# Kernel tuning notes

Measured on AMD Instinct MI355X. Metric: run time of the kernel, lower is better.

Reference implementation:

```python
import jax, jax.numpy as jnp
import numpy as np

EPS = 1e-5
NEG_SLOPE = 0.2


def batchnorm_nodes(x, gamma, beta):
    # BatchNorm2d over channel=node axis; x: [N, T, D], stats over (T, D) per node
    m = x.mean(axis=(1, 2), keepdims=True)
    v = ((x - m) ** 2).mean(axis=(1, 2), keepdims=True)
    return (x - m) * jax.lax.rsqrt(v + EPS) * gamma[:, None, None] + beta[:, None, None]


def gat_relation(h, src, dst, W, al, ar, N):
    # h: [N, T, D]; W: [D, H, dh]; al/ar: [H, dh]
    z = jnp.einsum('ntd,dhe->nthe', h, W)              # [N, T, H, dh]
    el = jnp.einsum('nthe,he->nth', z, al)             # [N, T, H]
    er = jnp.einsum('nthe,he->nth', z, ar)
    e = jax.nn.leaky_relu(el[src] + er[dst], NEG_SLOPE)  # [E, T, H]
    emax = jax.ops.segment_max(e, dst, num_segments=N)   # [N, T, H]
    ex = jnp.exp(e - emax[dst])
    denom = jax.ops.segment_sum(ex, dst, num_segments=N)
    alpha = ex / jnp.maximum(denom[dst], 1e-16)          # segment softmax over in-edges
    msg = alpha[..., None] * z[src]                      # [E, T, H, dh]
    return jax.ops.segment_sum(msg, dst, num_segments=N)  # [N, T, H, dh]


def setup_inputs() -> dict:
    key = jax.random.key(0)
    ks = jax.random.split(key, 12)
    N, T, D, H, E, DFF = 10000, 12, 64, 4, 100000, 128
    dh = D // H
    s = 0.1
    return {
        'x': jax.random.normal(ks[0], (N, T, D), jnp.float32),
        'src1': jax.random.randint(ks[1], (E,), 0, N, jnp.int32),
        'dst1': jax.random.randint(ks[2], (E,), 0, N, jnp.int32),
        'src2': jax.random.randint(ks[3], (E,), 0, N, jnp.int32),
        'dst2': jax.random.randint(ks[4], (E,), 0, N, jnp.int32),
        'W1': jax.random.normal(ks[5], (D, H, dh), jnp.float32) * s,
        'al1': jax.random.normal(ks[6], (H, dh), jnp.float32) * s,
        'ar1': jax.random.normal(ks[7], (H, dh), jnp.float32) * s,
        'W2': jax.random.normal(ks[8], (D, H, dh), jnp.float32) * s,
        'al2': jax.random.normal(ks[9], (H, dh), jnp.float32) * s,
        'ar2': jax.random.normal(ks[10], (H, dh), jnp.float32) * s,
        'bn1_g': jnp.ones((N,), jnp.float32),
        'bn1_b': jnp.zeros((N,), jnp.float32),
        'bn2_g': jnp.ones((N,), jnp.float32),
        'bn2_b': jnp.zeros((N,), jnp.float32),
        'ff_w1': jax.random.normal(ks[11], (D, DFF), jnp.float32) * s,
        'ff_b1': jnp.zeros((DFF,), jnp.float32),
        'ff_w2': jax.random.normal(jax.random.fold_in(key, 99), (DFF, D), jnp.float32) * s,
        'ff_b2': jnp.zeros((D,), jnp.float32),
    }


def reference(x, src1, dst1, src2, dst2, W1, al1, ar1, W2, al2, ar2,
              bn1_g, bn1_b, bn2_g, bn2_b, ff_w1, ff_b1, ff_w2, ff_b2):
    N, T, D = x.shape
    h = batchnorm_nodes(x, bn1_g, bn1_b)
    # HeteroGraphConv: per-relation GAT, sum aggregation
    m = gat_relation(h, src1, dst1, W1, al1, ar1, N) \
      + gat_relation(h, src2, dst2, W2, al2, ar2, N)   # [N, T, H, dh]
    m = m.reshape(N, T, D)
    x2 = x + m                                          # residual (dropout=identity in eval)
    h2 = batchnorm_nodes(x2, bn2_g, bn2_b)
    ff = jax.nn.gelu(h2 @ ff_w1 + ff_b1, approximate=False) @ ff_w2 + ff_b2
    return x2 + ff
```

## Files before the change

kernel.cpp:

```cpp
#include <hip/hip_runtime.h>
#include <math.h>

constexpr int kT = 12;
constexpr float kNeg = 0.2f;
constexpr float kEps = 1e-5f;
constexpr float kLog2e = 1.44269504088896f;

typedef __attribute__((ext_vector_type(8))) short bf16x8;
typedef __attribute__((ext_vector_type(4))) float f32x4;

__device__ __forceinline__ short f2bf(float f) {
  union { float f; unsigned u; } v;
  v.f = f;
  return (short)((v.u + 0x7fffu + ((v.u >> 16) & 1u)) >> 16);
}
__device__ __forceinline__ unsigned pack2(float a, float b) {
  return (unsigned)(unsigned short)f2bf(a) | ((unsigned)(unsigned short)f2bf(b) << 16);
}

__device__ __forceinline__ float wave_reduce_sum(float v) {
#pragma unroll
  for (int o = 32; o > 0; o >>= 1) v += __shfl_xor(v, o);
  return v;
}

__global__ void bnprep_kernel(const float* __restrict__ x, const float* __restrict__ g,
                              const float* __restrict__ b, float* __restrict__ scale,
                              float* __restrict__ shift, const float* __restrict__ fw1,
                              const float* __restrict__ fw2, const float* __restrict__ zW1,
                              const float* __restrict__ zW2, bf16x8* __restrict__ fw1f,
                              bf16x8* __restrict__ fw2f, bf16x8* __restrict__ zw1f,
                              bf16x8* __restrict__ zw2f, int N) {
  int blk = blockIdx.x;
  int lane = threadIdx.x & 63, wid = threadIdx.x >> 6;
  if (blk >= N) {
    int which = blk - N;
    int m = lane & 15, q = lane >> 4;
    if (which == 0) {
      for (int fi = wid; fi < 16; fi += 4) {
        int mt = fi >> 1, kc = fi & 1;
        bf16x8 v;
#pragma unroll
        for (int j = 0; j < 8; j++) v[j] = f2bf(fw1[(kc * 32 + q * 8 + j) * 128 + mt * 16 + m]);
        fw1f[fi * 64 + lane] = v;
      }
    } else if (which == 1) {
      for (int fi = wid; fi < 16; fi += 4) {
        int mt2 = fi >> 2, kc2 = fi & 3;
        bf16x8 u;
#pragma unroll
        for (int j = 0; j < 8; j++) u[j] = f2bf(fw2[(kc2 * 32 + q * 8 + j) * 64 + mt2 * 16 + m]);
        fw2f[fi * 64 + lane] = u;
      }
    } else if (which == 2) {
      for (int fi = wid; fi < 8; fi += 4) {
        int mt = fi >> 1, kc = fi & 1;
        bf16x8 v;
#pragma unroll
        for (int j = 0; j < 8; j++) v[j] = f2bf(zW1[(kc * 32 + q * 8 + j) * 64 + mt * 16 + m]);
        zw1f[fi * 64 + lane] = v;
      }
    } else {
      for (int fi = wid; fi < 8; fi += 4) {
        int mt = fi >> 1, kc = fi & 1;
        bf16x8 v;
#pragma unroll
        for (int j = 0; j < 8; j++) v[j] = f2bf(zW2[(kc * 32 + q * 8 + j) * 64 + mt * 16 + m]);
        zw2f[fi * 64 + lane] = v;
      }
    }
    return;
  }
  int n = blk;
  const float* xr = x + (size_t)n * (kT * 64);
  float s = 0.f, s2 = 0.f;
  for (int i = threadIdx.x; i < kT * 64; i += blockDim.x) {
    float v = xr[i];
    s += v;
    s2 += v * v;
  }
  s = wave_reduce_sum(s);
  s2 = wave_reduce_sum(s2);
  __shared__ float ls[4], ls2[4];
  if (lane == 0) { ls[wid] = s; ls2[wid] = s2; }
  __syncthreads();
  if (threadIdx.x == 0) {
    float ts = 0.f, ts2 = 0.f;
    for (int i = 0; i < 4; i++) { ts += ls[i]; ts2 += ls2[i]; }
    const float inv = 1.f / (kT * 64);
    float mean = ts * inv;
    float var = ts2 * inv - mean * mean;
    float sc = rsqrtf(var + kEps) * g[n];
    scale[n] = sc;
    shift[n] = b[n] - mean * sc;
  }
}

__global__ void deg_kernel(const int* __restrict__ dst1, const int* __restrict__ dst2,
                           int* __restrict__ deg1, int* __restrict__ deg2, int E1, int E2) {
  int i = blockIdx.x * blockDim.x + threadIdx.x;
  if (i < E1) atomicAdd(&deg1[dst1[i]], 1);
  else if (i < E1 + E2) atomicAdd(&deg2[dst2[i - E1]], 1);
}

__global__ void scan_kernel(const int* __restrict__ deg1, int* __restrict__ off1,
                            const int* __restrict__ deg2, int* __restrict__ off2, int N) {
  const int* deg = blockIdx.x ? deg2 : deg1;
  int* off = blockIdx.x ? off2 : off1;
  __shared__ int wsum[16];
  __shared__ int carry;
  int tid = threadIdx.x, lane = tid & 63, wv = tid >> 6;
  if (tid == 0) { carry = 0; off[0] = 0; }
  __syncthreads();
  for (int base = 0; base < N; base += 1024) {
    int i = base + tid;
    int incl = (i < N) ? deg[i] : 0;
#pragma unroll
    for (int o = 1; o < 64; o <<= 1) {
      int y = __shfl_up(incl, o);
      if (lane >= o) incl += y;
    }
    if (lane == 63) wsum[wv] = incl;
    __syncthreads();
    if (tid < 16) {
      int p = wsum[tid];
#pragma unroll
      for (int o = 1; o < 16; o <<= 1) {
        int y = __shfl_up(p, o);
        if (tid >= o) p += y;
      }
      wsum[tid] = p;
    }
    __syncthreads();
    int prefix = carry + (wv > 0 ? wsum[wv - 1] : 0);
    if (i < N) off[i + 1] = prefix + incl;
    int total = carry + wsum[15];
    __syncthreads();
    if (tid == 0) carry = total;
    __syncthreads();
  }
}

__global__ void fill_kernel(const int* __restrict__ src1, const int* __restrict__ dst1,
                            const int* __restrict__ off1, int* __restrict__ cur1,
                            int* __restrict__ scsr1, const int* __restrict__ src2,
                            const int* __restrict__ dst2, const int* __restrict__ off2,
                            int* __restrict__ cur2, int* __restrict__ scsr2, int E1, int E2) {
  int i = blockIdx.x * blockDim.x + threadIdx.x;
  if (i < E1) {
    int d = dst1[i];
    int p = atomicAdd(&cur1[d], 1);
    scsr1[off1[d] + p] = src1[i] * kT;
  } else if (i < E1 + E2) {
    int k = i - E1;
    int d = dst2[k];
    int p = atomicAdd(&cur2[d], 1);
    scsr2[off2[d] + p] = src2[k] * kT;
  }
}

__global__ __launch_bounds__(256) void zel_kernel(
    const float* __restrict__ x, const float* __restrict__ scale,
    const float* __restrict__ shift, const bf16x8* __restrict__ zw1f,
    const bf16x8* __restrict__ zw2f, const float* __restrict__ al1,
    const float* __restrict__ ar1, const float* __restrict__ al2,
    const float* __restrict__ ar2, unsigned short* __restrict__ z1,
    unsigned short* __restrict__ z2, float* __restrict__ el1, float* __restrict__ er1,
    float* __restrict__ el2, float* __restrict__ er2, int NT) {
  __shared__ bf16x8 sW1[8][64];
  __shared__ bf16x8 sW2[8][64];
  int lane = threadIdx.x & 63, wid = threadIdx.x >> 6;
  int m = lane & 15, q = lane >> 4;
  for (int fi = wid; fi < 8; fi += 4) {
    sW1[fi][lane] = zw1f[fi * 64 + lane];
    sW2[fi][lane] = zw2f[fi * 64 + lane];
  }
  __syncthreads();
  float al1r[4][4], ar1r[4][4], al2r[4][4], ar2r[4][4];
#pragma unroll
  for (int h = 0; h < 4; h++)
#pragma unroll
    for (int r = 0; r < 4; r++) {
      int f = h * 16 + 4 * q + r;
      al1r[h][r] = al1[f] * kLog2e;
      ar1r[h][r] = ar1[f] * kLog2e;
      al2r[h][r] = al2[f] * kLog2e;
      ar2r[h][r] = ar2[f] * kLog2e;
    }
  int ntile = (NT + 15) / 16;
  for (int tile = blockIdx.x * 4 + wid; tile < ntile; tile += gridDim.x * 4) {
    int r0 = tile * 16;
    int row = r0 + m;
    int rowc = (row < NT) ? row : NT - 1;
    int n = rowc / kT;
    float sc = scale[n], sh = shift[n];
    bf16x8 hf[2];
#pragma unroll
    for (int kc = 0; kc < 2; kc++) {
      float4 p0 = *(const float4*)&x[(size_t)rowc * 64 + kc * 32 + q * 8];
      float4 p1 = *(const float4*)&x[(size_t)rowc * 64 + kc * 32 + q * 8 + 4];
      hf[kc][0] = f2bf(fmaf(p0.x, sc, sh));
      hf[kc][1] = f2bf(fmaf(p0.y, sc, sh));
      hf[kc][2] = f2bf(fmaf(p0.z, sc, sh));
      hf[kc][3] = f2bf(fmaf(p0.w, sc, sh));
      hf[kc][4] = f2bf(fmaf(p1.x, sc, sh));
      hf[kc][5] = f2bf(fmaf(p1.y, sc, sh));
      hf[kc][6] = f2bf(fmaf(p1.z, sc, sh));
      hf[kc][7] = f2bf(fmaf(p1.w, sc, sh));
    }
    f32x4 a1[4], a2[4];
#pragma unroll
    for (int mt = 0; mt < 4; mt++) {
      a1[mt] = (f32x4){0.f, 0.f, 0.f, 0.f};
      a2[mt] = (f32x4){0.f, 0.f, 0.f, 0.f};
    }
#pragma unroll
    for (int kc = 0; kc < 2; kc++)
#pragma unroll
      for (int mt = 0; mt < 4; mt++) {
        a1[mt] = __builtin_amdgcn_mfma_f32_16x16x32_bf16(sW1[mt * 2 + kc][lane], hf[kc],
                                                         a1[mt], 0, 0, 0);
        a2[mt] = __builtin_amdgcn_mfma_f32_16x16x32_bf16(sW2[mt * 2 + kc][lane], hf[kc],
                                                         a2[mt], 0, 0, 0);
      }
    float e1l[4], e1r[4], e2l[4], e2r[4];
#pragma unroll
    for (int h = 0; h < 4; h++) {
      float pl1 = 0.f, pr1 = 0.f, pl2 = 0.f, pr2 = 0.f;
#pragma unroll
      for (int r = 0; r < 4; r++) {
        pl1 = fmaf(a1[h][r], al1r[h][r], pl1);
        pr1 = fmaf(a1[h][r], ar1r[h][r], pr1);
        pl2 = fmaf(a2[h][r], al2r[h][r], pl2);
        pr2 = fmaf(a2[h][r], ar2r[h][r], pr2);
      }
#pragma unroll
      for (int o = 16; o < 64; o <<= 1) {
        pl1 += __shfl_xor(pl1, o);
        pr1 += __shfl_xor(pr1, o);
        pl2 += __shfl_xor(pl2, o);
        pr2 += __shfl_xor(pr2, o);
      }
      e1l[h] = pl1; e1r[h] = pr1; e2l[h] = pl2; e2r[h] = pr2;
    }
    if (row < NT) {
      if (q == 0) {
        *(float4*)&el1[(size_t)row * 4] = make_float4(e1l[0], e1l[1], e1l[2], e1l[3]);
        *(float4*)&er1[(size_t)row * 4] = make_float4(e1r[0], e1r[1], e1r[2], e1r[3]);
        *(float4*)&el2[(size_t)row * 4] = make_float4(e2l[0], e2l[1], e2l[2], e2l[3]);
        *(float4*)&er2[(size_t)row * 4] = make_float4(e2r[0], e2r[1], e2r[2], e2r[3]);
      }
#pragma unroll
      for (int mt = 0; mt < 4; mt++) {
        uint2 u1 = {pack2(a1[mt][0], a1[mt][1]), pack2(a1[mt][2], a1[mt][3])};
        uint2 u2 = {pack2(a2[mt][0], a2[mt][1]), pack2(a2[mt][2], a2[mt][3])};
        *(uint2*)&z1[(size_t)row * 64 + mt * 16 + 4 * q] = u1;
        *(uint2*)&z2[(size_t)row * 64 + mt * 16 + 4 * q] = u2;
      }
    }
  }
}

__device__ __forceinline__ void gat_rel(int n, int t, const int* __restrict__ scsr,
                                        const int* __restrict__ off,
                                        const float* __restrict__ elp, float er_h,
                                        const unsigned short* __restrict__ zp, int lane,
                                        float& a0, float& a1, float& a2, float& a3) {
  int b0 = off[n], b1 = off[n + 1];
  if (b1 <= b0) return;
  float den = 0.f, n0 = 0.f, n1 = 0.f, n2 = 0.f, n3 = 0.f;
  for (int c0 = b0; c0 < b1; c0 += 64) {
    int cnt = b1 - c0;
    if (cnt > 64) cnt = 64;
    int idx = c0 + lane;
    int sbl = scsr[(idx < b1) ? idx : b1 - 1];
    int s0 = __shfl(sbl, 0) + t;
    int s1 = (cnt > 1) ? (__shfl(sbl, 1) + t) : s0;
    float e0 = elp[(size_t)s0 * 4];
    uint2 zz0 = *(const uint2*)(zp + (size_t)s0 * 64);
    float e1 = elp[(size_t)s1 * 4];
    uint2 zz1 = *(const uint2*)(zp + (size_t)s1 * 64);
    for (int k = 0; k < cnt; k++) {
      int s2 = (k + 2 < cnt) ? (__shfl(sbl, k + 2) + t) : s1;
      float e2 = elp[(size_t)s2 * 4];
      uint2 zz2 = *(const uint2*)(zp + (size_t)s2 * 64);
      float ev = e0 + er_h;
      ev = fmaxf(ev, kNeg * ev);
      float wgt = exp2f(ev);
      den += wgt;
      n0 = fmaf(wgt, __uint_as_float(zz0.x << 16), n0);
      n1 = fmaf(wgt, __uint_as_float(zz0.x & 0xffff0000u), n1);
      n2 = fmaf(wgt, __uint_as_float(zz0.y << 16), n2);
      n3 = fmaf(wgt, __uint_as_float(zz0.y & 0xffff0000u), n3);
      s0 = s1; e0 = e1; zz0 = zz1;
      s1 = s2; e1 = e2; zz1 = zz2;
    }
  }
  float inv = 1.f / den;
  a0 = fmaf(n0, inv, a0);
  a1 = fmaf(n1, inv, a1);
  a2 = fmaf(n2, inv, a2);
  a3 = fmaf(n3, inv, a3);
}

__global__ __launch_bounds__(256) void agg_kernel(
    const float* __restrict__ x, const int* __restrict__ scsr1,
    const int* __restrict__ off1, const float* __restrict__ el1,
    const float* __restrict__ er1, const unsigned short* __restrict__ z1,
    const int* __restrict__ scsr2, const int* __restrict__ off2,
    const float* __restrict__ el2, const float* __restrict__ er2,
    const unsigned short* __restrict__ z2, float* __restrict__ x2,
    float* __restrict__ bn2s, float* __restrict__ bn2q, int N) {
  int wid = threadIdx.x >> 6, lane = threadIdx.x & 63;
  int w = blockIdx.x * 4 + wid;
  if (w >= N * 3) return;
  int n = w / 3;
  int t0 = (w - n * 3) * 4;
  int tl = lane >> 4, cg = lane & 15;
  int t = t0 + tl;
  int row = n * kT + t;
  int h = cg >> 2;
  float a0 = 0.f, a1 = 0.f, a2 = 0.f, a3 = 0.f;
  gat_rel(n, t, scsr1, off1, el1 + h, er1[(size_t)row * 4 + h], z1 + cg * 4, lane, a0, a1, a2,
          a3);
  gat_rel(n, t, scsr2, off2, el2 + h, er2[(size_t)row * 4 + h], z2 + cg * 4, lane, a0, a1, a2,
          a3);

  size_t base = (size_t)row * 64 + cg * 4;
  float4 xr = *(const float4*)&x[base];
  float4 o;
  o.x = xr.x + a0;
  o.y = xr.y + a1;
  o.z = xr.z + a2;
  o.w = xr.w + a3;
  *(float4*)&x2[base] = o;
  float s1 = o.x + o.y + o.z + o.w;
  float s2 = o.x * o.x + o.y * o.y + o.z * o.z + o.w * o.w;
  s1 = wave_reduce_sum(s1);
  s2 = wave_reduce_sum(s2);
  if (lane == 0) {
    atomicAdd(&bn2s[n], s1);
    atomicAdd(&bn2q[n], s2);
  }
}

__global__ __launch_bounds__(256, 2) void ff_kernel(
    const float* __restrict__ x2, const float* __restrict__ bn2s,
    const float* __restrict__ bn2q, const float* __restrict__ bng,
    const float* __restrict__ bnb, const bf16x8* __restrict__ w1f,
    const bf16x8* __restrict__ w2f, const float* __restrict__ b1,
    const float* __restrict__ b2, float* __restrict__ out, int NT) {
  __shared__ bf16x8 sW1[16][64];
  __shared__ bf16x8 sW2[16][64];
  __shared__ float sB1[128];
  __shared__ float sB2[64];
  int lane = threadIdx.x & 63, wid = threadIdx.x >> 6;
  int m = lane & 15, q = lane >> 4;
  {
    int fi0 = wid * 4;
#pragma unroll
    for (int k = 0; k < 4; k++) {
      sW1[fi0 + k][lane] = w1f[(fi0 + k) * 64 + lane];
      sW2[fi0 + k][lane] = w2f[(fi0 + k) * 64 + lane];
    }
    if (threadIdx.x < 128) sB1[threadIdx.x] = b1[threadIdx.x];
    if (threadIdx.x < 64) sB2[threadIdx.x] = b2[threadIdx.x];
  }
  __syncthreads();

  const float inv = 1.f / (kT * 64);
  int ntile = (NT + 15) / 16;
  for (int tile = blockIdx.x * 4 + wid; tile < ntile; tile += gridDim.x * 4) {
    int r0 = tile * 16;
    int row = r0 + m;
    int rowc = (row < NT) ? row : NT - 1;
    int n = rowc / kT;
    float mean = bn2s[n] * inv;
    float var = bn2q[n] * inv - mean * mean;
    float sc = rsqrtf(var + kEps) * bng[n];
    float sh = bnb[n] - mean * sc;

    bf16x8 hf[2];
#pragma unroll
    for (int kc = 0; kc < 2; kc++) {
      const float4 p0 = *(const float4*)&x2[(size_t)rowc * 64 + kc * 32 + q * 8];
      const float4 p1 = *(const float4*)&x2[(size_t)rowc * 64 + kc * 32 + q * 8 + 4];
      hf[kc][0] = f2bf(fmaf(p0.x, sc, sh));
      hf[kc][1] = f2bf(fmaf(p0.y, sc, sh));
      hf[kc][2] = f2bf(fmaf(p0.z, sc, sh));
      hf[kc][3] = f2bf(fmaf(p0.w, sc, sh));
      hf[kc][4] = f2bf(fmaf(p1.x, sc, sh));
      hf[kc][5] = f2bf(fmaf(p1.y, sc, sh));
      hf[kc][6] = f2bf(fmaf(p1.z, sc, sh));
      hf[kc][7] = f2bf(fmaf(p1.w, sc, sh));
    }

    f32x4 acc[8];
#pragma unroll
    for (int mt = 0; mt < 8; mt++) acc[mt] = (f32x4){0.f, 0.f, 0.f, 0.f};
#pragma unroll
    for (int kc = 0; kc < 2; kc++)
#pragma unroll
      for (int mt = 0; mt < 8; mt++)
        acc[mt] = __builtin_amdgcn_mfma_f32_16x16x32_bf16(sW1[mt * 2 + kc][lane], hf[kc],
                                                          acc[mt], 0, 0, 0);

    f32x4 acc2[4];
#pragma unroll
    for (int mt = 0; mt < 4; mt++) acc2[mt] = (f32x4){0.f, 0.f, 0.f, 0.f};
#pragma unroll
    for (int kc = 0; kc < 4; kc++) {
      float4 bb0 = *(const float4*)&sB1[(2 * kc) * 16 + 4 * q];
      float4 bb1 = *(const float4*)&sB1[(2 * kc + 1) * 16 + 4 * q];
      float g0[4], g1[4];
      {
        float u;
        u = acc[2 * kc][0] + bb0.x; g0[0] = 0.5f * u * (1.f + erff(u * 0.70710678118654752f));
        u = acc[2 * kc][1] + bb0.y; g0[1] = 0.5f * u * (1.f + erff(u * 0.70710678118654752f));
        u = acc[2 * kc][2] + bb0.z; g0[2] = 0.5f * u * (1.f + erff(u * 0.70710678118654752f));
        u = acc[2 * kc][3] + bb0.w; g0[3] = 0.5f * u * (1.f + erff(u * 0.70710678118654752f));
        u = acc[2 * kc + 1][0] + bb1.x; g1[0] = 0.5f * u * (1.f + erff(u * 0.70710678118654752f));
        u = acc[2 * kc + 1][1] + bb1.y; g1[1] = 0.5f * u * (1.f + erff(u * 0.70710678118654752f));
        u = acc[2 * kc + 1][2] + bb1.z; g1[2] = 0.5f * u * (1.f + erff(u * 0.70710678118654752f));
        u = acc[2 * kc + 1][3] + bb1.w; g1[3] = 0.5f * u * (1.f + erff(u * 0.70710678118654752f));
      }
      bf16x8 bf;
#pragma unroll
      for (int j = 0; j < 8; j++) {
        int srcq = (2 * q + (j >> 2)) & 3;
        int src = srcq * 16 + m;
        float v0 = __shfl(g0[j & 3], src);
        float v1 = __shfl(g1[j & 3], src);
        bf[j] = f2bf((q >= 2) ? v1 : v0);
      }
#pragma unroll
      for (int mt = 0; mt < 4; mt++)
        acc2[mt] = __builtin_amdgcn_mfma_f32_16x16x32_bf16(sW2[mt * 4 + kc][lane], bf,
                                                           acc2[mt], 0, 0, 0);
    }

    if (row < NT) {
#pragma unroll
      for (int mt = 0; mt < 4; mt++) {
        size_t base = (size_t)row * 64 + mt * 16 + 4 * q;
        float4 xr = *(const float4*)&x2[base];
        float4 bb = *(const float4*)&sB2[mt * 16 + 4 * q];
        float4 o;
        o.x = acc2[mt][0] + bb.x + xr.x;
        o.y = acc2[mt][1] + bb.y + xr.y;
        o.z = acc2[mt][2] + bb.z + xr.z;
        o.w = acc2[mt][3] + bb.w + xr.w;
        *(float4*)&out[base] = o;
      }
    }
  }
}

extern "C" void kernel_launch(void* const* d_in, const int* in_sizes, int n_in,
                              void* d_out, int out_size, void* d_ws, size_t ws_size,
                              hipStream_t stream) {
  const float* x = (const float*)d_in[0];
  const int* src1 = (const int*)d_in[1];
  const int* dst1 = (const int*)d_in[2];
  const int* src2 = (const int*)d_in[3];
  const int* dst2 = (const int*)d_in[4];
  const float* W1 = (const float*)d_in[5];
  const float* al1 = (const float*)d_in[6];
  const float* ar1 = (const float*)d_in[7];
  const float* W2 = (const float*)d_in[8];
  const float* al2 = (const float*)d_in[9];
  const float* ar2 = (const float*)d_in[10];
  const float* g1 = (const float*)d_in[11];
  const float* b1 = (const float*)d_in[12];
  const float* g2 = (const float*)d_in[13];
  const float* b2 = (const float*)d_in[14];
  const float* fw1 = (const float*)d_in[15];
  const float* fb1 = (const float*)d_in[16];
  const float* fw2 = (const float*)d_in[17];
  const float* fb2 = (const float*)d_in[18];

  const int N = in_sizes[11];
  const int E1 = in_sizes[1];
  const int E2 = in_sizes[3];
  const int NT = N * kT;

  char* p = (char*)d_ws;
  auto alloc = [&](size_t bytes) -> char* {
    char* r = p;
    p += (bytes + 255) & ~(size_t)255;
    return r;
  };
  unsigned short* z1 = (unsigned short*)alloc((size_t)NT * 64 * 2);
  unsigned short* z2 = (unsigned short*)alloc((size_t)NT * 64 * 2);
  float* el1 = (float*)alloc((size_t)NT * 4 * 4);
  float* er1 = (float*)alloc((size_t)NT * 4 * 4);
  float* el2 = (float*)alloc((size_t)NT * 4 * 4);
  float* er2 = (float*)alloc((size_t)NT * 4 * 4);
  float* x2 = (float*)alloc((size_t)NT * 64 * 4);
  float* sc1 = (float*)alloc((size_t)N * 4);
  float* sh1 = (float*)alloc((size_t)N * 4);
  int* off1 = (int*)alloc((size_t)(N + 1) * 4);
  int* off2 = (int*)alloc((size_t)(N + 1) * 4);
  int* scsr1 = (int*)alloc((size_t)E1 * 4);
  int* scsr2 = (int*)alloc((size_t)E2 * 4);
  bf16x8* fw1f = (bf16x8*)alloc(16 * 64 * 16);
  bf16x8* fw2f = (bf16x8*)alloc(16 * 64 * 16);
  bf16x8* zw1f = (bf16x8*)alloc(8 * 64 * 16);
  bf16x8* zw2f = (bf16x8*)alloc(8 * 64 * 16);
  char* zero_base = p;
  int* deg1 = (int*)alloc((size_t)N * 4);
  int* cur1 = (int*)alloc((size_t)N * 4);
  int* deg2 = (int*)alloc((size_t)N * 4);
  int* cur2 = (int*)alloc((size_t)N * 4);
  float* bn2s = (float*)alloc((size_t)N * 4);
  float* bn2q = (float*)alloc((size_t)N * 4);
  size_t zero_bytes = (size_t)(p - zero_base);
  hipMemsetAsync(zero_base, 0, zero_bytes, stream);

  bnprep_kernel<<<N + 4, 256, 0, stream>>>(x, g1, b1, sc1, sh1, fw1, fw2, W1, W2, fw1f, fw2f,
                                           zw1f, zw2f, N);
  deg_kernel<<<(E1 + E2 + 255) / 256, 256, 0, stream>>>(dst1, dst2, deg1, deg2, E1, E2);
  scan_kernel<<<2, 1024, 0, stream>>>(deg1, off1, deg2, off2, N);
  fill_kernel<<<(E1 + E2 + 255) / 256, 256, 0, stream>>>(src1, dst1, off1, cur1, scsr1, src2,
                                                         dst2, off2, cur2, scsr2, E1, E2);
  zel_kernel<<<1875, 256, 0, stream>>>(x, sc1, sh1, zw1f, zw2f, al1, ar1, al2, ar2, z1, z2,
                                       el1, er1, el2, er2, NT);
  agg_kernel<<<(N * 3 + 3) / 4, 256, 0, stream>>>(x, scsr1, off1, el1, er1, z1, scsr2, off2,
                                                  el2, er2, z2, x2, bn2s, bn2q, N);
  ff_kernel<<<1875, 256, 0, stream>>>(x2, bn2s, bn2q, g2, b2, fw1f, fw2f, fb1, fb2,
                                      (float*)d_out, NT);
}
```

Baseline: 268.4 us.

## Fuse prep kernels, fold attention vectors into weights, deepen prefetch, two-tile FF

Several changes at once. BN statistics, weight packing and degree counting now run in one prep kernel with one wave per node, and CSR fill runs in the same launch as the z/el projection. The attention vectors al/ar are folded into the projection weights (W·a) so el/er come from one extra MFMA instead of shuffle reductions. The aggregation gather prefetch is deepened from two to three edges ahead, and the FF kernel handles two 16-row tiles per wave to reuse weight fragments. Together these cut launch count and per-tile overhead, at the cost of higher register pressure and a different rounding path for el/er, which are now computed from bf16-rounded folded weights.

```diff
diff --git a/kernel.cpp b/kernel.cpp
--- a/kernel.cpp
+++ b/kernel.cpp
@@ -24,81 +24,106 @@
   return v;
 }
 
-__global__ void bnprep_kernel(const float* __restrict__ x, const float* __restrict__ g,
-                              const float* __restrict__ b, float* __restrict__ scale,
-                              float* __restrict__ shift, const float* __restrict__ fw1,
-                              const float* __restrict__ fw2, const float* __restrict__ zW1,
-                              const float* __restrict__ zW2, bf16x8* __restrict__ fw1f,
-                              bf16x8* __restrict__ fw2f, bf16x8* __restrict__ zw1f,
-                              bf16x8* __restrict__ zw2f, int N) {
+__global__ void prep_kernel(const float* __restrict__ x, const float* __restrict__ g,
+                            const float* __restrict__ b, float* __restrict__ scale,
+                            float* __restrict__ shift, const float* __restrict__ fw1,
+                            const float* __restrict__ fw2, const float* __restrict__ zW1,
+                            const float* __restrict__ zW2, const float* __restrict__ al1,
+                            const float* __restrict__ ar1, const float* __restrict__ al2,
+                            const float* __restrict__ ar2, bf16x8* __restrict__ fw1f,
+                            bf16x8* __restrict__ fw2f, bf16x8* __restrict__ zw1f,
+                            bf16x8* __restrict__ zw2f, bf16x8* __restrict__ walf,
+                            const int* __restrict__ dst1, const int* __restrict__ dst2,
+                            int* __restrict__ deg1, int* __restrict__ deg2, int N, int E1,
+                            int E2, int nBnBlk) {
   int blk = blockIdx.x;
   int lane = threadIdx.x & 63, wid = threadIdx.x >> 6;
-  if (blk >= N) {
-    int which = blk - N;
-    int m = lane & 15, q = lane >> 4;
-    if (which == 0) {
-      for (int fi = wid; fi < 16; fi += 4) {
-        int mt = fi >> 1, kc = fi & 1;
+  if (blk < nBnBlk) {
+    int n = blk * 4 + wid;
+    if (n < N) {
+      const float* xr = x + (size_t)n * 768;
+      float s = 0.f, s2 = 0.f;
+#pragma unroll
+      for (int c = 0; c < 3; c++) {
+        float4 v = *(const float4*)&xr[c * 256 + lane * 4];
+        s += v.x + v.y + v.z + v.w;
+        s2 += v.x * v.x + v.y * v.y + v.z * v.z + v.w * v.w;
+      }
+      s = wave_reduce_sum(s);
+      s2 = wave_reduce_sum(s2);
+      if (lane == 0) {
+        const float inv = 1.f / 768.f;
+        float mean = s * inv;
+        float var = s2 * inv - mean * mean;
+        float sc = rsqrtf(var + kEps) * g[n];
+        scale[n] = sc;
+        shift[n] = b[n] - mean * sc;
+      }
+    }
+    return;
+  }
+  blk -= nBnBlk;
+  int m = lane & 15, q = lane >> 4;
+  if (blk == 0) {
+    for (int fi = wid; fi < 16; fi += 4) {
+      int mt = fi >> 1, kc = fi & 1;
+      bf16x8 v;
+#pragma unroll
+      for (int j = 0; j < 8; j++) v[j] = f2bf(fw1[(kc * 32 + q * 8 + j) * 128 + mt * 16 + m]);
+      fw1f[fi * 64 + lane] = v;
+    }
+    return;
+  }
+  if (blk == 1) {
+    for (int fi = wid; fi < 16; fi += 4) {
+      int mt2 = fi >> 2, kc2 = fi & 3;
+      bf16x8 u;
+#pragma unroll
+      for (int j = 0; j < 8; j++) u[j] = f2bf(fw2[(kc2 * 32 + q * 8 + j) * 64 + mt2 * 16 + m]);
+      fw2f[fi * 64 + lane] = u;
+    }
+    return;
+  }
+  if (blk == 2) {
+    for (int fi = wid; fi < 8; fi += 4) {
+      int mt = fi >> 1, kc = fi & 1;
+      bf16x8 v, u;
+#pragma unroll
+      for (int j = 0; j < 8; j++) {
+        int d = kc * 32 + q * 8 + j;
+        v[j] = f2bf(zW1[d * 64 + mt * 16 + m]);
+        u[j] = f2bf(zW2[d * 64 + mt * 16 + m]);
+      }
+      zw1f[fi * 64 + lane] = v;
+      zw2f[fi * 64 + lane] = u;
+    }
+    return;
+  }
+  if (blk == 3) {
+    __shared__ float wal[16][64];
+    for (int e0 = threadIdx.x; e0 < 1024; e0 += 256) {
+      int f = e0 >> 6, d = e0 & 63;
+      int h = f & 3;
+      const float* av = (f < 4) ? al1 : (f < 8) ? ar1 : (f < 12) ? al2 : ar2;
+      const float* W = (f < 8) ? zW1 : zW2;
+      float s = 0.f;
+#pragma unroll
+      for (int e = 0; e < 16; e++) s += W[d * 64 + h * 16 + e] * av[h * 16 + e];
+      wal[f][d] = s * kLog2e;
+    }
+    __syncthreads();
+    if (wid == 0) {
+#pragma unroll
+      for (int kc = 0; kc < 2; kc++) {
         bf16x8 v;
 #pragma unroll
-        for (int j = 0; j < 8; j++) v[j] = f2bf(fw1[(kc * 32 + q * 8 + j) * 128 + mt * 16 + m]);
-        fw1f[fi * 64 + lane] = v;
-      }
-    } else if (which == 1) {
-      for (int fi = wid; fi < 16; fi += 4) {
-        int mt2 = fi >> 2, kc2 = fi & 3;
-        bf16x8 u;
-#pragma unroll
-        for (int j = 0; j < 8; j++) u[j] = f2bf(fw2[(kc2 * 32 + q * 8 + j) * 64 + mt2 * 16 + m]);
-        fw2f[fi * 64 + lane] = u;
-      }
-    } else if (which == 2) {
-      for (int fi = wid; fi < 8; fi += 4) {
-        int mt = fi >> 1, kc = fi & 1;
-        bf16x8 v;
-#pragma unroll
-        for (int j = 0; j < 8; j++) v[j] = f2bf(zW1[(kc * 32 + q * 8 + j) * 64 + mt * 16 + m]);
-        zw1f[fi * 64 + lane] = v;
-      }
-    } else {
-      for (int fi = wid; fi < 8; fi += 4) {
-        int mt = fi >> 1, kc = fi & 1;
-        bf16x8 v;
-#pragma unroll
-        for (int j = 0; j < 8; j++) v[j] = f2bf(zW2[(kc * 32 + q * 8 + j) * 64 + mt * 16 + m]);
-        zw2f[fi * 64 + lane] = v;
+        for (int j = 0; j < 8; j++) v[j] = f2bf(wal[m][kc * 32 + q * 8 + j]);
+        walf[kc * 64 + lane] = v;
       }
     }
     return;
   }
-  int n = blk;
-  const float* xr = x + (size_t)n * (kT * 64);
-  float s = 0.f, s2 = 0.f;
-  for (int i = threadIdx.x; i < kT * 64; i += blockDim.x) {
-    float v = xr[i];
-    s += v;
-    s2 += v * v;
-  }
-  s = wave_reduce_sum(s);
-  s2 = wave_reduce_sum(s2);
-  __shared__ float ls[4], ls2[4];
-  if (lane == 0) { ls[wid] = s; ls2[wid] = s2; }
-  __syncthreads();
-  if (threadIdx.x == 0) {
-    float ts = 0.f, ts2 = 0.f;
-    for (int i = 0; i < 4; i++) { ts += ls[i]; ts2 += ls2[i]; }
-    const float inv = 1.f / (kT * 64);
-    float mean = ts * inv;
-    float var = ts2 * inv - mean * mean;
-    float sc = rsqrtf(var + kEps) * g[n];
-    scale[n] = sc;
-    shift[n] = b[n] - mean * sc;
-  }
-}
-
-__global__ void deg_kernel(const int* __restrict__ dst1, const int* __restrict__ dst2,
-                           int* __restrict__ deg1, int* __restrict__ deg2, int E1, int E2) {
-  int i = blockIdx.x * blockDim.x + threadIdx.x;
+  int i = (blk - 4) * 256 + threadIdx.x;
   if (i < E1) atomicAdd(&deg1[dst1[i]], 1);
   else if (i < E1 + E2) atomicAdd(&deg2[dst2[i - E1]], 1);
 }
@@ -141,54 +166,47 @@
   }
 }
 
-__global__ void fill_kernel(const int* __restrict__ src1, const int* __restrict__ dst1,
-                            const int* __restrict__ off1, int* __restrict__ cur1,
-                            int* __restrict__ scsr1, const int* __restrict__ src2,
-                            const int* __restrict__ dst2, const int* __restrict__ off2,
-                            int* __restrict__ cur2, int* __restrict__ scsr2, int E1, int E2) {
-  int i = blockIdx.x * blockDim.x + threadIdx.x;
-  if (i < E1) {
-    int d = dst1[i];
-    int p = atomicAdd(&cur1[d], 1);
-    scsr1[off1[d] + p] = src1[i] * kT;
-  } else if (i < E1 + E2) {
-    int k = i - E1;
-    int d = dst2[k];
-    int p = atomicAdd(&cur2[d], 1);
-    scsr2[off2[d] + p] = src2[k] * kT;
-  }
-}
-
-__global__ __launch_bounds__(256) void zel_kernel(
+__global__ __launch_bounds__(256) void fillzel_kernel(
+    const int* __restrict__ src1, const int* __restrict__ dst1, const int* __restrict__ off1,
+    int* __restrict__ cur1, int* __restrict__ scsr1, const int* __restrict__ src2,
+    const int* __restrict__ dst2, const int* __restrict__ off2, int* __restrict__ cur2,
+    int* __restrict__ scsr2, int E1, int E2, int nZelBlk,
     const float* __restrict__ x, const float* __restrict__ scale,
     const float* __restrict__ shift, const bf16x8* __restrict__ zw1f,
-    const bf16x8* __restrict__ zw2f, const float* __restrict__ al1,
-    const float* __restrict__ ar1, const float* __restrict__ al2,
-    const float* __restrict__ ar2, unsigned short* __restrict__ z1,
-    unsigned short* __restrict__ z2, float* __restrict__ el1, float* __restrict__ er1,
-    float* __restrict__ el2, float* __restrict__ er2, int NT) {
+    const bf16x8* __restrict__ zw2f, const bf16x8* __restrict__ walf,
+    unsigned short* __restrict__ z1, unsigned short* __restrict__ z2,
+    float* __restrict__ el1, float* __restrict__ er1, float* __restrict__ el2,
+    float* __restrict__ er2, int NT) {
+  if ((int)blockIdx.x >= nZelBlk) {
+    int i = ((int)blockIdx.x - nZelBlk) * 256 + threadIdx.x;
+    if (i < E1) {
+      int d = dst1[i];
+      int p = atomicAdd(&cur1[d], 1);
+      scsr1[off1[d] + p] = src1[i] * kT;
+    } else if (i < E1 + E2) {
+      int k = i - E1;
+      int d = dst2[k];
+      int p = atomicAdd(&cur2[d], 1);
+      scsr2[off2[d] + p] = src2[k] * kT;
+    }
+    return;
+  }
   __shared__ bf16x8 sW1[8][64];
   __shared__ bf16x8 sW2[8][64];
+  __shared__ bf16x8 sWE[2][64];
   int lane = threadIdx.x & 63, wid = threadIdx.x >> 6;
   int m = lane & 15, q = lane >> 4;
   for (int fi = wid; fi < 8; fi += 4) {
     sW1[fi][lane] = zw1f[fi * 64 + lane];
     sW2[fi][lane] = zw2f[fi * 64 + lane];
   }
+  if (wid == 0) {
+    sWE[0][lane] = walf[lane];
+    sWE[1][lane] = walf[64 + lane];
+  }
   __syncthreads();
-  float al1r[4][4], ar1r[4][4], al2r[4][4], ar2r[4][4];
-#pragma unroll
-  for (int h = 0; h < 4; h++)
-#pragma unroll
-    for (int r = 0; r < 4; r++) {
-      int f = h * 16 + 4 * q + r;
-      al1r[h][r] = al1[f] * kLog2e;
-      ar1r[h][r] = ar1[f] * kLog2e;
-      al2r[h][r] = al2[f] * kLog2e;
-      ar2r[h][r] = ar2[f] * kLog2e;
-    }
   int ntile = (NT + 15) / 16;
-  for (int tile = blockIdx.x * 4 + wid; tile < ntile; tile += gridDim.x * 4) {
+  for (int tile = blockIdx.x * 4 + wid; tile < ntile; tile += nZelBlk * 4) {
     int r0 = tile * 16;
     int row = r0 + m;
     int rowc = (row < NT) ? row : NT - 1;
@@ -208,14 +226,15 @@
       hf[kc][6] = f2bf(fmaf(p1.z, sc, sh));
       hf[kc][7] = f2bf(fmaf(p1.w, sc, sh));
     }
-    f32x4 a1[4], a2[4];
+    f32x4 a1[4], a2[4], ae;
 #pragma unroll
     for (int mt = 0; mt < 4; mt++) {
       a1[mt] = (f32x4){0.f, 0.f, 0.f, 0.f};
       a2[mt] = (f32x4){0.f, 0.f, 0.f, 0.f};
     }
-#pragma unroll
-    for (int kc = 0; kc < 2; kc++)
+    ae = (f32x4){0.f, 0.f, 0.f, 0.f};
+#pragma unroll
+    for (int kc = 0; kc < 2; kc++) {
 #pragma unroll
       for (int mt = 0; mt < 4; mt++) {
         a1[mt] = __builtin_amdgcn_mfma_f32_16x16x32_bf16(sW1[mt * 2 + kc][lane], hf[kc],
@@ -223,33 +242,11 @@
         a2[mt] = __builtin_amdgcn_mfma_f32_16x16x32_bf16(sW2[mt * 2 + kc][lane], hf[kc],
                                                          a2[mt], 0, 0, 0);
       }
-    float e1l[4], e1r[4], e2l[4], e2r[4];
-#pragma unroll
-    for (int h = 0; h < 4; h++) {
-      float pl1 = 0.f, pr1 = 0.f, pl2 = 0.f, pr2 = 0.f;
-#pragma unroll
-      for (int r = 0; r < 4; r++) {
-        pl1 = fmaf(a1[h][r], al1r[h][r], pl1);
-        pr1 = fmaf(a1[h][r], ar1r[h][r], pr1);
-        pl2 = fmaf(a2[h][r], al2r[h][r], pl2);
-        pr2 = fmaf(a2[h][r], ar2r[h][r], pr2);
-      }
-#pragma unroll
-      for (int o = 16; o < 64; o <<= 1) {
-        pl1 += __shfl_xor(pl1, o);
-        pr1 += __shfl_xor(pr1, o);
-        pl2 += __shfl_xor(pl2, o);
-        pr2 += __shfl_xor(pr2, o);
-      }
-      e1l[h] = pl1; e1r[h] = pr1; e2l[h] = pl2; e2r[h] = pr2;
+      ae = __builtin_amdgcn_mfma_f32_16x16x32_bf16(sWE[kc][lane], hf[kc], ae, 0, 0, 0);
     }
     if (row < NT) {
-      if (q == 0) {
-        *(float4*)&el1[(size_t)row * 4] = make_float4(e1l[0], e1l[1], e1l[2], e1l[3]);
-        *(float4*)&er1[(size_t)row * 4] = make_float4(e1r[0], e1r[1], e1r[2], e1r[3]);
-        *(float4*)&el2[(size_t)row * 4] = make_float4(e2l[0], e2l[1], e2l[2], e2l[3]);
-        *(float4*)&er2[(size_t)row * 4] = make_float4(e2r[0], e2r[1], e2r[2], e2r[3]);
-      }
+      float* edst = (q == 0) ? el1 : (q == 1) ? er1 : (q == 2) ? el2 : er2;
+      *(float4*)&edst[(size_t)row * 4] = make_float4(ae[0], ae[1], ae[2], ae[3]);
 #pragma unroll
       for (int mt = 0; mt < 4; mt++) {
         uint2 u1 = {pack2(a1[mt][0], a1[mt][1]), pack2(a1[mt][2], a1[mt][3])};
@@ -276,24 +273,28 @@
     int sbl = scsr[(idx < b1) ? idx : b1 - 1];
     int s0 = __shfl(sbl, 0) + t;
     int s1 = (cnt > 1) ? (__shfl(sbl, 1) + t) : s0;
+    int s2 = (cnt > 2) ? (__shfl(sbl, 2) + t) : s1;
     float e0 = elp[(size_t)s0 * 4];
-    uint2 zz0 = *(const uint2*)(zp + (size_t)s0 * 64);
+    uint2 z0 = *(const uint2*)(zp + (size_t)s0 * 64);
     float e1 = elp[(size_t)s1 * 4];
     uint2 zz1 = *(const uint2*)(zp + (size_t)s1 * 64);
+    float e2 = elp[(size_t)s2 * 4];
+    uint2 zz2 = *(const uint2*)(zp + (size_t)s2 * 64);
     for (int k = 0; k < cnt; k++) {
-      int s2 = (k + 2 < cnt) ? (__shfl(sbl, k + 2) + t) : s1;
-      float e2 = elp[(size_t)s2 * 4];
-      uint2 zz2 = *(const uint2*)(zp + (size_t)s2 * 64);
+      int s3 = (k + 3 < cnt) ? (__shfl(sbl, k + 3) + t) : s2;
+      float e3 = elp[(size_t)s3 * 4];
+      uint2 zz3 = *(const uint2*)(zp + (size_t)s3 * 64);
       float ev = e0 + er_h;
       ev = fmaxf(ev, kNeg * ev);
       float wgt = exp2f(ev);
       den += wgt;
-      n0 = fmaf(wgt, __uint_as_float(zz0.x << 16), n0);
-      n1 = fmaf(wgt, __uint_as_float(zz0.x & 0xffff0000u), n1);
-      n2 = fmaf(wgt, __uint_as_float(zz0.y << 16), n2);
-      n3 = fmaf(wgt, __uint_as_float(zz0.y & 0xffff0000u), n3);
-      s0 = s1; e0 = e1; zz0 = zz1;
+      n0 = fmaf(wgt, __uint_as_float(z0.x << 16), n0);
+      n1 = fmaf(wgt, __uint_as_float(z0.x & 0xffff0000u), n1);
+      n2 = fmaf(wgt, __uint_as_float(z0.y << 16), n2);
+      n3 = fmaf(wgt, __uint_as_float(z0.y & 0xffff0000u), n3);
+      s0 = s1; e0 = e1; z0 = zz1;
       s1 = s2; e1 = e2; zz1 = zz2;
+      s2 = s3; e2 = e3; zz2 = zz3;
     }
   }
   float inv = 1.f / den;
@@ -368,77 +369,89 @@
   }
   __syncthreads();
 
-  const float inv = 1.f / (kT * 64);
-  int ntile = (NT + 15) / 16;
-  for (int tile = blockIdx.x * 4 + wid; tile < ntile; tile += gridDim.x * 4) {
-    int r0 = tile * 16;
-    int row = r0 + m;
+  const float inv = 1.f / 768.f;
+  int grp = blockIdx.x * 4 + wid;
+  int ngrp = (NT + 31) / 32;
+  if (grp >= ngrp) return;
+
+  bf16x8 hf[2][2];
+  f32x4 acc[2][8];
+#pragma unroll
+  for (int tt = 0; tt < 2; tt++) {
+    int row = grp * 32 + tt * 16 + m;
     int rowc = (row < NT) ? row : NT - 1;
     int n = rowc / kT;
     float mean = bn2s[n] * inv;
     float var = bn2q[n] * inv - mean * mean;
     float sc = rsqrtf(var + kEps) * bng[n];
     float sh = bnb[n] - mean * sc;
-
-    bf16x8 hf[2];
 #pragma unroll
     for (int kc = 0; kc < 2; kc++) {
       const float4 p0 = *(const float4*)&x2[(size_t)rowc * 64 + kc * 32 + q * 8];
       const float4 p1 = *(const float4*)&x2[(size_t)rowc * 64 + kc * 32 + q * 8 + 4];
-      hf[kc][0] = f2bf(fmaf(p0.x, sc, sh));
-      hf[kc][1] = f2bf(fmaf(p0.y, sc, sh));
-      hf[kc][2] = f2bf(fmaf(p0.z, sc, sh));
-      hf[kc][3] = f2bf(fmaf(p0.w, sc, sh));
-      hf[kc][4] = f2bf(fmaf(p1.x, sc, sh));
-      hf[kc][5] = f2bf(fmaf(p1.y, sc, sh));
-      hf[kc][6] = f2bf(fmaf(p1.z, sc, sh));
-      hf[kc][7] = f2bf(fmaf(p1.w, sc, sh));
-    }
-
-    f32x4 acc[8];
-#pragma unroll
-    for (int mt = 0; mt < 8; mt++) acc[mt] = (f32x4){0.f, 0.f, 0.f, 0.f};
-#pragma unroll
-    for (int kc = 0; kc < 2; kc++)
-#pragma unroll
-      for (int mt = 0; mt < 8; mt++)
-        acc[mt] = __builtin_amdgcn_mfma_f32_16x16x32_bf16(sW1[mt * 2 + kc][lane], hf[kc],
-                                                          acc[mt], 0, 0, 0);
-
-    f32x4 acc2[4];
-#pragma unroll
-    for (int mt = 0; mt < 4; mt++) acc2[mt] = (f32x4){0.f, 0.f, 0.f, 0.f};
-#pragma unroll
-    for (int kc = 0; kc < 4; kc++) {
-      float4 bb0 = *(const float4*)&sB1[(2 * kc) * 16 + 4 * q];
-      float4 bb1 = *(const float4*)&sB1[(2 * kc + 1) * 16 + 4 * q];
+      hf[tt][kc][0] = f2bf(fmaf(p0.x, sc, sh));
+      hf[tt][kc][1] = f2bf(fmaf(p0.y, sc, sh));
+      hf[tt][kc][2] = f2bf(fmaf(p0.z, sc, sh));
+      hf[tt][kc][3] = f2bf(fmaf(p0.w, sc, sh));
+      hf[tt][kc][4] = f2bf(fmaf(p1.x, sc, sh));
+      hf[tt][kc][5] = f2bf(fmaf(p1.y, sc, sh));
+      hf[tt][kc][6] = f2bf(fmaf(p1.z, sc, sh));
+      hf[tt][kc][7] = f2bf(fmaf(p1.w, sc, sh));
+    }
+#pragma unroll
+    for (int mt = 0; mt < 8; mt++) acc[tt][mt] = (f32x4){0.f, 0.f, 0.f, 0.f};
+  }
+#pragma unroll
+  for (int kc = 0; kc < 2; kc++)
+#pragma unroll
+    for (int mt = 0; mt < 8; mt++)
+#pragma unroll
+      for (int tt = 0; tt < 2; tt++)
+        acc[tt][mt] = __builtin_amdgcn_mfma_f32_16x16x32_bf16(sW1[mt * 2 + kc][lane],
+                                                              hf[tt][kc], acc[tt][mt], 0, 0, 0);
+
+  f32x4 acc2[2][4];
+#pragma unroll
+  for (int tt = 0; tt < 2; tt++)
+#pragma unroll
+    for (int mt = 0; mt < 4; mt++) acc2[tt][mt] = (f32x4){0.f, 0.f, 0.f, 0.f};
+#pragma unroll
+  for (int kc = 0; kc < 4; kc++) {
+    float4 bb0 = *(const float4*)&sB1[(2 * kc) * 16 + 4 * q];
+    float4 bb1 = *(const float4*)&sB1[(2 * kc + 1) * 16 + 4 * q];
+    bf16x8 bf[2];
+#pragma unroll
+    for (int tt = 0; tt < 2; tt++) {
       float g0[4], g1[4];
-      {
-        float u;
-        u = acc[2 * kc][0] + bb0.x; g0[0] = 0.5f * u * (1.f + erff(u * 0.70710678118654752f));
-        u = acc[2 * kc][1] + bb0.y; g0[1] = 0.5f * u * (1.f + erff(u * 0.70710678118654752f));
-        u = acc[2 * kc][2] + bb0.z; g0[2] = 0.5f * u * (1.f + erff(u * 0.70710678118654752f));
-        u = acc[2 * kc][3] + bb0.w; g0[3] = 0.5f * u * (1.f + erff(u * 0.70710678118654752f));
-        u = acc[2 * kc + 1][0] + bb1.x; g1[0] = 0.5f * u * (1.f + erff(u * 0.70710678118654752f));
-        u = acc[2 * kc + 1][1] + bb1.y; g1[1] = 0.5f * u * (1.f + erff(u * 0.70710678118654752f));
-        u = acc[2 * kc + 1][2] + bb1.z; g1[2] = 0.5f * u * (1.f + erff(u * 0.70710678118654752f));
-        u = acc[2 * kc + 1][3] + bb1.w; g1[3] = 0.5f * u * (1.f + erff(u * 0.70710678118654752f));
-      }
-      bf16x8 bf;
+      float u;
+      u = acc[tt][2 * kc][0] + bb0.x; g0[0] = 0.5f * u * (1.f + erff(u * 0.70710678118654752f));
+      u = acc[tt][2 * kc][1] + bb0.y; g0[1] = 0.5f * u * (1.f + erff(u * 0.70710678118654752f));
+      u = acc[tt][2 * kc][2] + bb0.z; g0[2] = 0.5f * u * (1.f + erff(u * 0.70710678118654752f));
+      u = acc[tt][2 * kc][3] + bb0.w; g0[3] = 0.5f * u * (1.f + erff(u * 0.70710678118654752f));
+      u = acc[tt][2 * kc + 1][0] + bb1.x; g1[0] = 0.5f * u * (1.f + erff(u * 0.70710678118654752f));
+      u = acc[tt][2 * kc + 1][1] + bb1.y; g1[1] = 0.5f * u * (1.f + erff(u * 0.70710678118654752f));
+      u = acc[tt][2 * kc + 1][2] + bb1.z; g1[2] = 0.5f * u * (1.f + erff(u * 0.70710678118654752f));
+      u = acc[tt][2 * kc + 1][3] + bb1.w; g1[3] = 0.5f * u * (1.f + erff(u * 0.70710678118654752f));
 #pragma unroll
       for (int j = 0; j < 8; j++) {
         int srcq = (2 * q + (j >> 2)) & 3;
         int src = srcq * 16 + m;
         float v0 = __shfl(g0[j & 3], src);
         float v1 = __shfl(g1[j & 3], src);
-        bf[j] = f2bf((q >= 2) ? v1 : v0);
-      }
-#pragma unroll
-      for (int mt = 0; mt < 4; mt++)
-        acc2[mt] = __builtin_amdgcn_mfma_f32_16x16x32_bf16(sW2[mt * 4 + kc][lane], bf,
-                                                           acc2[mt], 0, 0, 0);
-    }
-
+        bf[tt][j] = f2bf((q >= 2) ? v1 : v0);
+      }
+    }
+#pragma unroll
+    for (int mt = 0; mt < 4; mt++)
+#pragma unroll
+      for (int tt = 0; tt < 2; tt++)
+        acc2[tt][mt] = __builtin_amdgcn_mfma_f32_16x16x32_bf16(sW2[mt * 4 + kc][lane], bf[tt],
+                                                               acc2[tt][mt], 0, 0, 0);
+  }
+
+#pragma unroll
+  for (int tt = 0; tt < 2; tt++) {
+    int row = grp * 32 + tt * 16 + m;
     if (row < NT) {
 #pragma unroll
       for (int mt = 0; mt < 4; mt++) {
@@ -446,10 +459,10 @@
         float4 xr = *(const float4*)&x2[base];
         float4 bb = *(const float4*)&sB2[mt * 16 + 4 * q];
         float4 o;
-        o.x = acc2[mt][0] + bb.x + xr.x;
-        o.y = acc2[mt][1] + bb.y + xr.y;
-        o.z = acc2[mt][2] + bb.z + xr.z;
-        o.w = acc2[mt][3] + bb.w + xr.w;
+        o.x = acc2[tt][mt][0] + bb.x + xr.x;
+        o.y = acc2[tt][mt][1] + bb.y + xr.y;
+        o.z = acc2[tt][mt][2] + bb.z + xr.z;
+        o.w = acc2[tt][mt][3] + bb.w + xr.w;
         *(float4*)&out[base] = o;
       }
     }
@@ -507,6 +520,7 @@
   bf16x8* fw2f = (bf16x8*)alloc(16 * 64 * 16);
   bf16x8* zw1f = (bf16x8*)alloc(8 * 64 * 16);
   bf16x8* zw2f = (bf16x8*)alloc(8 * 64 * 16);
+  bf16x8* walf = (bf16x8*)alloc(2 * 64 * 16);
   char* zero_base = p;
   int* deg1 = (int*)alloc((size_t)N * 4);
   int* cur1 = (int*)alloc((size_t)N * 4);
@@ -517,16 +531,18 @@
   size_t zero_bytes = (size_t)(p - zero_base);
   hipMemsetAsync(zero_base, 0, zero_bytes, stream);
 
-  bnprep_kernel<<<N + 4, 256, 0, stream>>>(x, g1, b1, sc1, sh1, fw1, fw2, W1, W2, fw1f, fw2f,
-                                           zw1f, zw2f, N);
-  deg_kernel<<<(E1 + E2 + 255) / 256, 256, 0, stream>>>(dst1, dst2, deg1, deg2, E1, E2);
+  const int nBnBlk = (N + 3) / 4;
+  const int degBlk = (E1 + E2 + 255) / 256;
+  prep_kernel<<<nBnBlk + 4 + degBlk, 256, 0, stream>>>(
+      x, g1, b1, sc1, sh1, fw1, fw2, W1, W2, al1, ar1, al2, ar2, fw1f, fw2f, zw1f, zw2f, walf,
+      dst1, dst2, deg1, deg2, N, E1, E2, nBnBlk);
   scan_kernel<<<2, 1024, 0, stream>>>(deg1, off1, deg2, off2, N);
-  fill_kernel<<<(E1 + E2 + 255) / 256, 256, 0, stream>>>(src1, dst1, off1, cur1, scsr1, src2,
-                                                         dst2, off2, cur2, scsr2, E1, E2);
-  zel_kernel<<<1875, 256, 0, stream>>>(x, sc1, sh1, zw1f, zw2f, al1, ar1, al2, ar2, z1, z2,
-                                       el1, er1, el2, er2, NT);
+  const int nZelBlk = 1875;
+  fillzel_kernel<<<nZelBlk + degBlk, 256, 0, stream>>>(
+      src1, dst1, off1, cur1, scsr1, src2, dst2, off2, cur2, scsr2, E1, E2, nZelBlk, x, sc1,
+      sh1, zw1f, zw2f, walf, z1, z2, el1, er1, el2, er2, NT);
   agg_kernel<<<(N * 3 + 3) / 4, 256, 0, stream>>>(x, scsr1, off1, el1, er1, z1, scsr2, off2,
                                                   el2, er2, z2, x2, bn2s, bn2q, N);
-  ff_kernel<<<1875, 256, 0, stream>>>(x2, bn2s, bn2q, g2, b2, fw1f, fw2f, fb1, fb2,
-                                      (float*)d_out, NT);
-}
+  ff_kernel<<<((NT + 31) / 32 + 3) / 4, 256, 0, stream>>>(x2, bn2s, bn2q, g2, b2, fw1f, fw2f,
+                                                          fb1, fb2, (float*)d_out, NT);
+}
```

Result: faster. 252.5 us (-5.9%).
